# Performance work log

Hardware: AMD Instinct MI355X
Metric: run time of the kernel (lower is better)

Reference implementation:

```python
import jax, jax.numpy as jnp
import numpy as np
from jax import lax

B, SQ, SK, D, K = 4, 2048, 2048, 1024, 3


def setup_inputs() -> dict:
    key = jax.random.key(0)
    ks = jax.random.split(key, 16)
    s = 0.02
    return {
        "query_hidden": jax.random.normal(ks[0], (B, SQ, D), jnp.float32),
        "memory_hidden": jax.random.normal(ks[1], (B, SK, D), jnp.float32),
        "attention_mask": jax.random.randint(ks[2], (SQ, SK), 0, 2).astype(bool),
        # Linear projections (torch: y = x @ W.T + b)
        "q_w": jax.random.normal(ks[3], (D, D), jnp.float32) * s,
        "q_b": jnp.zeros((D,), jnp.float32),
        "k_w": jax.random.normal(ks[4], (D, D), jnp.float32) * s,
        "k_b": jnp.zeros((D,), jnp.float32),
        "v_w": jax.random.normal(ks[5], (D, D), jnp.float32) * s,
        "v_b": jnp.zeros((D,), jnp.float32),
        "o_w": jax.random.normal(ks[6], (D, D), jnp.float32) * s,
        "o_b": jnp.zeros((D,), jnp.float32),
        # ConvTransform1D: depthwise conv kernels [D,1,K], bias [D], scalar gate
        "q_kernel": jax.random.normal(ks[7], (D, 1, K), jnp.float32) * s,
        "q_cbias": jnp.zeros((D,), jnp.float32),
        "q_gate": jnp.zeros((), jnp.float32),
        "k_kernel": jax.random.normal(ks[8], (D, 1, K), jnp.float32) * s,
        "k_cbias": jnp.zeros((D,), jnp.float32),
        "k_gate": jnp.zeros((), jnp.float32),
        "v_kernel": jax.random.normal(ks[9], (D, 1, K), jnp.float32) * s,
        "v_cbias": jnp.zeros((D,), jnp.float32),
        "v_gate": jnp.zeros((), jnp.float32),
    }


def _conv_transform(x, kernel, cbias, gate):
    """Gated depthwise 1D conv along seq: x + tanh(gate) * dwconv(x). x: [B,S,D]."""
    xc = jnp.transpose(x, (0, 2, 1))  # [B,D,S]
    y = lax.conv_general_dilated(
        xc, kernel, window_strides=(1,), padding="SAME",
        dimension_numbers=("NCH", "OIH", "NCH"), feature_group_count=x.shape[-1])
    y = y + cbias[None, :, None]
    return x + jnp.tanh(gate) * jnp.transpose(y, (0, 2, 1))


def reference(query_hidden, memory_hidden, attention_mask,
              q_w, q_b, k_w, k_b, v_w, v_b, o_w, o_b,
              q_kernel, q_cbias, q_gate,
              k_kernel, k_cbias, k_gate,
              v_kernel, v_cbias, v_gate):
    d_model = query_hidden.shape[-1]
    q = _conv_transform(query_hidden @ q_w.T + q_b, q_kernel, q_cbias, q_gate)
    k = _conv_transform(memory_hidden @ k_w.T + k_b, k_kernel, k_cbias, k_gate)
    v = _conv_transform(memory_hidden @ v_w.T + v_b, v_kernel, v_cbias, v_gate)
    # [B,Sq,Sk]
    logits = jnp.einsum("bqd,bkd->bqk", q, k) / jnp.sqrt(jnp.float32(d_model))
    mask = attention_mask[None, :, :]  # broadcast like torch unsqueeze(0)
    logits = jnp.where(mask, logits, jnp.finfo(logits.dtype).min)
    attn = jax.nn.softmax(logits, axis=-1)
    out = jnp.einsum("bqk,bkd->bqd", attn, v) @ o_w.T + o_b
    return out
```

## Files before the change

### kernel.cpp

```cpp
#include <hip/hip_runtime.h>
#include <cstdint>
#include <cstddef>


#define GLOBAL_AS __attribute__((address_space(1)))
#define LDS_AS    __attribute__((address_space(3)))

typedef _Float16 h8 __attribute__((ext_vector_type(8)));
typedef float    f4_t __attribute__((ext_vector_type(4)));
typedef unsigned short us8 __attribute__((ext_vector_type(8)));

__device__ __forceinline__ float bf2f(unsigned short u) {
    union { unsigned int i; float f; } x; x.i = ((unsigned int)u) << 16; return x.f;
}
__device__ __forceinline__ float rd(const void* p, long i, int isBf) {
    return isBf ? bf2f(((const unsigned short*)p)[i]) : ((const float*)p)[i];
}

struct Probe16 { const unsigned short* p[16]; int n[16]; };

__global__ void k_probes(Probe16 a, const unsigned int* __restrict__ mask,
                         int* __restrict__ flags) {
    if (blockIdx.x < 16) {
        __shared__ int cnt;
        if (threadIdx.x == 0) cnt = 0;
        __syncthreads();
        const unsigned short* s = a.p[blockIdx.x];
        const int n = a.n[blockIdx.x];
        int bad = 0;
        for (int i = threadIdx.x; i < n; i += 256) {
            int e = (s[i] >> 7) & 0xFF;
            if (e >= 0x8F || (e > 0 && e <= 0x60)) bad++;
        }
        atomicAdd(&cnt, bad);
        __syncthreads();
        if (threadIdx.x == 0) flags[blockIdx.x] = (cnt * 4 > n) ? 0 : 1;
    } else {
        __shared__ int vi32, vf32, vbf, vf16;
        if (threadIdx.x == 0) { vi32 = vf32 = vbf = vf16 = 0; }
        __syncthreads();
        int bi32 = 0, bf32 = 0, bbf = 0, bf16c = 0;
        for (int i = threadIdx.x; i < 4096; i += 256) {
            unsigned int w = mask[i];
            if (!(w == 0u || w == 1u)) bi32++;
            if (!(w == 0u || w == 0x3F800000u)) bf32++;
            unsigned int h0 = w & 0xFFFFu, h1 = w >> 16;
            if (!((h0 == 0u || h0 == 0x3F80u) && (h1 == 0u || h1 == 0x3F80u))) bbf++;
            if (!((h0 == 0u || h0 == 0x3C00u) && (h1 == 0u || h1 == 0x3C00u))) bf16c++;
        }
        if (bi32) atomicAdd(&vi32, 1);
        if (bf32) atomicAdd(&vf32, 1);
        if (bbf)  atomicAdd(&vbf, 1);
        if (bf16c) atomicAdd(&vf16, 1);
        __syncthreads();
        if (threadIdx.x == 0) {
            int w;
            if (vi32 == 0) w = 4;
            else if (vf32 == 0) w = 4;
            else if (vbf == 0) w = 2;
            else if (vf16 == 0) w = 2;
            else w = 1;
            flags[16] = w;
        }
    }
}

__global__ void k_mask_bytes(const void* __restrict__ m, unsigned char* __restrict__ out,
                             long n, const int* __restrict__ widthFlag) {
    long i = ((long)blockIdx.x * 256 + threadIdx.x) * 4;
    if (i >= n) return;
    const int w = *widthFlag;
    unsigned int packed = 0;
    if (w == 4) {
        const unsigned int* p = (const unsigned int*)m;
#pragma unroll
        for (int u = 0; u < 4; ++u) packed |= (p[i + u] != 0u ? 1u : 0u) << (8 * u);
    } else if (w == 2) {
        const unsigned short* p = (const unsigned short*)m;
#pragma unroll
        for (int u = 0; u < 4; ++u) packed |= (p[i + u] != 0u ? 1u : 0u) << (8 * u);
    } else {
        const unsigned char* p = (const unsigned char*)m;
#pragma unroll
        for (int u = 0; u < 4; ++u) packed |= (p[i + u] != 0u ? 1u : 0u) << (8 * u);
    }
    *(unsigned int*)(out + i) = packed;
}

struct ConvSrc { const void* kern[3]; const void* cb[3]; const void* gate[3]; };
__global__ void k_conv_params(ConvSrc p, const int* __restrict__ flags,
                              _Float16* __restrict__ out, float* __restrict__ tg, int D) {
#pragma unroll
    for (int t = 0; t < 3; ++t) {
        const int kIs = flags[6 + t], cIs = flags[13 + t];
        for (int d = threadIdx.x; d < D; d += 256) {
#pragma unroll
            for (int j = 0; j < 3; ++j)
                out[t * 3 * D + j * D + d] = (_Float16)rd(p.kern[t], (long)d * 3 + j, kIs);
            out[9 * D + t * D + d] = (_Float16)rd(p.cb[t], d, cIs);
        }
    }
    if (threadIdx.x < 3) {
        const void* g = p.gate[threadIdx.x];
        float gv = rd(g, 0, ((const unsigned int*)g)[0] == 0u ? 1 : 0);
        tg[threadIdx.x] = tanhf(gv);
    }
}

__device__ __forceinline__ h8 cvt8(const void* src, size_t off8, int isBf) {
    h8 d;
    if (isBf) {
        us8 s = *(const us8*)((const unsigned short*)src + off8 * 8);
#pragma unroll
        for (int u = 0; u < 8; ++u) d[u] = (_Float16)bf2f(s[u]);
    } else {
        const float* f = (const float*)src + off8 * 8;
        f4_t a = *(const f4_t*)f;
        f4_t b = *(const f4_t*)(f + 4);
#pragma unroll
        for (int u = 0; u < 4; ++u) { d[u] = (_Float16)a[u]; d[4 + u] = (_Float16)b[u]; }
    }
    return d;
}

__global__ void k_h_to_f16(const void* __restrict__ s0, const void* __restrict__ s1,
                           _Float16* __restrict__ dst, int n8each,
                           const int* __restrict__ flags) {
    int i = blockIdx.x * blockDim.x + threadIdx.x;
    if (i >= 2 * n8each) return;
    int seg = i / n8each, off = i - seg * n8each;
    h8 d = cvt8(seg ? s1 : s0, off, flags[seg]);
    *(h8*)(dst + (size_t)i * 8) = d;
}

struct Ptr4 { const void* p[4]; };
__global__ void k_w_to_f16(Ptr4 srcs, _Float16* __restrict__ dst, int n8each,
                           const int* __restrict__ flags) {
    int i = blockIdx.x * blockDim.x + threadIdx.x;
    if (i >= 4 * n8each) return;
    int seg = i / n8each, off = i - seg * n8each;
    h8 d = cvt8(srcs.p[seg], off, flags[seg]);
    *(h8*)(dst + (size_t)i * 8) = d;
}

template <int MODE, int MTILE>
__global__ __launch_bounds__(256, 4) void k_gemm_nt(
    const _Float16* __restrict__ A, const _Float16* __restrict__ Bm,
    void* __restrict__ Cout,
    const void* __restrict__ bias, const int* __restrict__ biasFlag,
    const void* __restrict__ bias2, const int* __restrict__ biasFlag2,
    int N, int K, long sA, long sB, long sC,
    float scale, const unsigned char* __restrict__ mask8,
    int NT, int BZ) {

    constexpr int NI = (MTILE == 128) ? 4 : 2;
    constexpr int NCA = MTILE / 32;
    __shared__ __align__(16) _Float16 As[MTILE * 64];
    __shared__ __align__(16) _Float16 Bs[128 * 64];

    const long id = blockIdx.x;
    const int xcd = (int)(id & 7);
    const long local = id >> 3;
    const int col = (int)(local % NT);
    const long g = (local / NT) * 8 + xcd;
    const int bz = (int)(g % BZ);
    const int brow = (int)(g / BZ);

    const int tid  = threadIdx.x;
    const int wave = tid >> 6, lane = tid & 63;
    const int wm = (wave >> 1) * (MTILE / 2), wn = (wave & 1) * 64;
    const int lr = lane & 15, lq = lane >> 4;

    const _Float16* Ab = A + (long)bz * sA + (size_t)brow * MTILE * K;
    const _Float16* Bb = Bm + (long)bz * sB + (size_t)col * 128 * K;

    f4_t acc[NI][4] = {};

    const _Float16* gA[NCA];
    _Float16* lA[NCA];
#pragma unroll
    for (int j = 0; j < NCA; ++j) {
        int c = tid + j * 256;
        int r = c >> 3, s = ((c & 7) - r) & 7;
        gA[j] = Ab + (size_t)r * K + s * 8;
        lA[j] = As + c * 8;
    }
    const _Float16* gB[4];
    _Float16* lB[4];
#pragma unroll
    for (int j = 0; j < 4; ++j) {
        int c = tid + j * 256;
        int r = c >> 3, s = ((c & 7) - r) & 7;
        gB[j] = Bb + (size_t)r * K + s * 8;
        lB[j] = Bs + c * 8;
    }

    for (int kb = 0; kb < K; kb += 64) {
#pragma unroll
        for (int j = 0; j < NCA; ++j)
            __builtin_amdgcn_global_load_lds((void GLOBAL_AS*)(gA[j] + kb), (void LDS_AS*)lA[j], 16, 0, 0);
#pragma unroll
        for (int j = 0; j < 4; ++j)
            __builtin_amdgcn_global_load_lds((void GLOBAL_AS*)(gB[j] + kb), (void LDS_AS*)lB[j], 16, 0, 0);
        __syncthreads();

#pragma unroll
        for (int t = 0; t < 2; ++t) {
            const int fs = ((t * 4 + lq + lr) & 7) * 8;
            h8 af[NI], bfr[4];
#pragma unroll
            for (int i = 0; i < NI; ++i) af[i]  = *(const h8*)&As[(wm + i * 16 + lr) * 64 + fs];
#pragma unroll
            for (int j = 0; j < 4; ++j) bfr[j] = *(const h8*)&Bs[(wn + j * 16 + lr) * 64 + fs];
#pragma unroll
            for (int i = 0; i < NI; ++i)
#pragma unroll
                for (int j = 0; j < 4; ++j)
                    acc[i][j] = __builtin_amdgcn_mfma_f32_16x16x32_f16(af[i], bfr[j], acc[i][j], 0, 0, 0);
        }
        __syncthreads();
    }

    const long row0 = (long)brow * MTILE + wm + lq * 4;
    const long col0 = (long)col * 128 + wn + lr;

    if constexpr (MODE == 3) {
        _Float16* C = (_Float16*)Cout + (long)bz * sC;
#pragma unroll
        for (int i = 0; i < NI; ++i)
#pragma unroll
            for (int j = 0; j < 4; ++j)
#pragma unroll
                for (int r = 0; r < 4; ++r) {
                    long row = row0 + i * 16 + r;
                    long ccol = col0 + j * 16;
                    bool keep = mask8[row * (long)N + ccol] != 0;
                    float v = acc[i][j][r] * scale;
                    v = fminf(fmaxf(v, -60000.0f), 60000.0f);
                    C[row * (long)N + ccol] = (_Float16)(keep ? v : -60000.0f);
                }
    } else {
        float bv[4];
        if constexpr (MODE != 0) {
            const void* bp = bias; const int* bfp = biasFlag; long boff = 0;
            if (bias2 != nullptr && col * 128 >= (N >> 1)) {
                bp = bias2; bfp = biasFlag2; boff = (long)(N >> 1);
            }
            const int bIs = *bfp;
#pragma unroll
            for (int j = 0; j < 4; ++j) bv[j] = rd(bp, col0 + j * 16 - boff, bIs);
        } else {
#pragma unroll
            for (int j = 0; j < 4; ++j) bv[j] = 0.0f;
        }
        if constexpr (MODE == 2) {
            float* C = (float*)Cout + (long)bz * sC;
#pragma unroll
            for (int i = 0; i < NI; ++i)
#pragma unroll
                for (int j = 0; j < 4; ++j)
#pragma unroll
                    for (int r = 0; r < 4; ++r)
                        C[(row0 + i * 16 + r) * (long)N + col0 + j * 16] = acc[i][j][r] + bv[j];
        } else {
            _Float16* C = (_Float16*)Cout + (long)bz * sC;
#pragma unroll
            for (int i = 0; i < NI; ++i)
#pragma unroll
                for (int j = 0; j < 4; ++j)
#pragma unroll
                    for (int r = 0; r < 4; ++r) {
                        float v = acc[i][j][r] + bv[j];
                        v = fminf(fmaxf(v, -65000.0f), 65000.0f);
                        C[(row0 + i * 16 + r) * (long)N + col0 + j * 16] = (_Float16)v;
                    }
        }
    }
}

struct ConvP {
    const _Float16* x; int xs; _Float16* y;
    const _Float16* kp; const _Float16* cb; const float* tg;
};
__global__ void k_dwconv2(ConvP p0, ConvP p1, int S, int D) {
    const ConvP& p = blockIdx.z ? p1 : p0;
    int s = blockIdx.x, b = blockIdx.y;
    int d0 = threadIdx.x * 8;
    const size_t xb = ((size_t)b * S + s) * p.xs + d0;
    const size_t yb = ((size_t)b * S + s) * D + d0;
    h8 zero;
#pragma unroll
    for (int u = 0; u < 8; ++u) zero[u] = (_Float16)0.0f;
    h8 xc = *(const h8*)(p.x + xb);
    h8 xp = (s > 0)     ? *(const h8*)(p.x + xb - p.xs) : zero;
    h8 xn = (s < S - 1) ? *(const h8*)(p.x + xb + p.xs) : zero;
    h8 k0 = *(const h8*)(p.kp + 0 * D + d0);
    h8 k1 = *(const h8*)(p.kp + 1 * D + d0);
    h8 k2 = *(const h8*)(p.kp + 2 * D + d0);
    h8 cb = *(const h8*)(p.cb + d0);
    float tg = *p.tg;
    h8 o;
#pragma unroll
    for (int u = 0; u < 8; ++u) {
        float cv = (float)xp[u] * (float)k0[u] + (float)xc[u] * (float)k1[u] +
                   (float)xn[u] * (float)k2[u] + (float)cb[u];
        float v = (float)xc[u] + tg * cv;
        o[u] = (_Float16)fminf(fmaxf(v, -65000.0f), 65000.0f);
    }
    *(h8*)(p.y + yb) = o;
}

__global__ void k_dwconv_t(const _Float16* __restrict__ x, int xs,
                           _Float16* __restrict__ vt,
                           const _Float16* __restrict__ kp,
                           const _Float16* __restrict__ cbp,
                           const float* __restrict__ tgp,
                           int SK, int D) {
    __shared__ _Float16 T[64][65];
    int b = blockIdx.z;
    int s0 = blockIdx.x * 64, d0 = blockIdx.y * 64;
    int tid = threadIdx.x;
    float tg = *tgp;
    h8 zero;
#pragma unroll
    for (int u = 0; u < 8; ++u) zero[u] = (_Float16)0.0f;
#pragma unroll
    for (int it = 0; it < 2; ++it) {
        int idx = it * 256 + tid;
        int r = idx >> 3, c = (idx & 7) * 8;
        int s = s0 + r;
        const size_t xb = ((size_t)b * SK + s) * xs + d0 + c;
        h8 xc = *(const h8*)(x + xb);
        h8 xp = (s > 0)      ? *(const h8*)(x + xb - xs) : zero;
        h8 xn = (s < SK - 1) ? *(const h8*)(x + xb + xs) : zero;
        h8 k0 = *(const h8*)(kp + 0 * D + d0 + c);
        h8 k1 = *(const h8*)(kp + 1 * D + d0 + c);
        h8 k2 = *(const h8*)(kp + 2 * D + d0 + c);
        h8 cb = *(const h8*)(cbp + d0 + c);
#pragma unroll
        for (int u = 0; u < 8; ++u) {
            float cv = (float)xp[u] * (float)k0[u] + (float)xc[u] * (float)k1[u] +
                       (float)xn[u] * (float)k2[u] + (float)cb[u];
            float v = (float)xc[u] + tg * cv;
            T[r][c + u] = (_Float16)fminf(fmaxf(v, -65000.0f), 65000.0f);
        }
    }
    __syncthreads();
#pragma unroll
    for (int it = 0; it < 2; ++it) {
        int idx = it * 256 + tid;
        int dr = idx >> 3, c = (idx & 7) * 8;
        h8 o;
#pragma unroll
        for (int u = 0; u < 8; ++u) o[u] = T[c + u][dr];
        *(h8*)(vt + ((size_t)b * D + d0 + dr) * SK + s0 + c) = o;
    }
}

__global__ __launch_bounds__(256) void k_softmax(const _Float16* __restrict__ sc,
                                                 _Float16* __restrict__ pr, int SK) {
    const long row = blockIdx.x;
    const int tid = threadIdx.x, lane = tid & 63, wave = tid >> 6;
    h8 v = *(const h8*)(sc + row * (long)SK + tid * 8);
    float f[8]; float mx = -3.0e38f;
#pragma unroll
    for (int u = 0; u < 8; ++u) { f[u] = (float)v[u]; mx = fmaxf(mx, f[u]); }
#pragma unroll
    for (int o = 32; o > 0; o >>= 1) mx = fmaxf(mx, __shfl_xor(mx, o, 64));
    __shared__ float red[8];
    if (lane == 0) red[wave] = mx;
    __syncthreads();
    mx = fmaxf(fmaxf(red[0], red[1]), fmaxf(red[2], red[3]));
    float sum = 0.0f;
#pragma unroll
    for (int u = 0; u < 8; ++u) { f[u] = __expf(f[u] - mx); sum += f[u]; }
#pragma unroll
    for (int o = 32; o > 0; o >>= 1) sum += __shfl_xor(sum, o, 64);
    if (lane == 0) red[4 + wave] = sum;
    __syncthreads();
    sum = red[4] + red[5] + red[6] + red[7];
    float inv = 1.0f / sum;
    h8 o8;
#pragma unroll
    for (int u = 0; u < 8; ++u) o8[u] = (_Float16)(f[u] * inv);
    *(h8*)(pr + row * (long)SK + tid * 8) = o8;
}

extern "C" void kernel_launch(void* const* d_in, const int* in_sizes, int n_in,
                              void* d_out, int out_size, void* d_ws, size_t ws_size,
                              hipStream_t stream) {
    const int Bn = 4, SQ = 2048, SK = 2048, D = 1024;
    const size_t nQ = (size_t)Bn * SQ * D;
    const long   nM = (long)SQ * SK;

    const void* qh = d_in[0];
    const void* mh = d_in[1];
    const void* mask = d_in[2];
    const void* q_w = d_in[3];
    const void* q_b = d_in[4];
    const void* k_w = d_in[5];
    const void* k_b = d_in[6];
    const void* v_w = d_in[7];
    const void* v_b = d_in[8];
    const void* o_w = d_in[9];
    const void* o_b = d_in[10];
    const void* q_kern = d_in[11];
    const void* q_cb   = d_in[12];
    const void* q_g    = d_in[13];
    const void* k_kern = d_in[14];
    const void* k_cb   = d_in[15];
    const void* k_g    = d_in[16];
    const void* v_kern = d_in[17];
    const void* v_cb   = d_in[18];
    const void* v_g    = d_in[19];

    char* ws = (char*)d_ws;
    _Float16* scores   = (_Float16*)(ws + 0);
    _Float16* attn_out = (_Float16*)(ws + 0);
    _Float16* w16      = (_Float16*)(ws + 33554432);
    unsigned char* mask8 = (unsigned char*)(ws + 33554432);
    _Float16* par16    = (_Float16*)(ws + 37748736);
    float*    tgf      = (float*)(ws + 37748736 + 12 * 1024 * 2);
    _Float16* lin      = (_Float16*)(ws + 41943040);
    _Float16* lin_q    = lin;
    _Float16* lin_kv   = lin + nQ;
    _Float16* probs    = lin;
    _Float16* conv     = (_Float16*)(ws + 92274688);
    _Float16* qh16     = conv;
    _Float16* mh16     = conv + nQ;
    _Float16* vt       = (_Float16*)(ws + 125829120);
    int*      flags    = (int*)(ws + 142606336);

    Probe16 pa;
    const void* pp[16] = {qh, mh, q_w, k_w, v_w, o_w, q_kern, k_kern, v_kern,
                          q_b, k_b, v_b, o_b, q_cb, k_cb, v_cb};
    const int   pn[16] = {2048, 2048, 2048, 2048, 2048, 2048, 3072, 3072, 3072,
                          1024, 1024, 1024, 1024, 1024, 1024, 1024};
    for (int i = 0; i < 16; ++i) { pa.p[i] = (const unsigned short*)pp[i]; pa.n[i] = pn[i]; }
    k_probes<<<17, 256, 0, stream>>>(pa, (const unsigned int*)mask, flags);

    const int nH8 = (int)(nQ / 8);
    k_h_to_f16<<<(2 * nH8 + 255) / 256, 256, 0, stream>>>(qh, mh, qh16, nH8, flags + 0);
    const int nW8 = D * D / 8;
    Ptr4 wp; wp.p[0] = q_w; wp.p[1] = k_w; wp.p[2] = v_w; wp.p[3] = o_w;
    k_w_to_f16<<<(4 * nW8 + 255) / 256, 256, 0, stream>>>(wp, w16, nW8, flags + 2);

    k_gemm_nt<1, 64><<<dim3(1024), 256, 0, stream>>>(
        qh16, w16, lin_q, q_b, flags + 9, nullptr, nullptr,
        D, D, 0, 0, 0, 1.0f, nullptr, 8, 1);
    k_gemm_nt<1, 128><<<dim3(1024), 256, 0, stream>>>(
        mh16, w16 + (size_t)D * D, lin_kv, k_b, flags + 10, v_b, flags + 11,
        2 * D, D, 0, 0, 0, 1.0f, nullptr, 16, 1);

    k_mask_bytes<<<(int)(nM / 4 / 256), 256, 0, stream>>>(mask, mask8, nM, flags + 16);
    ConvSrc cs;
    cs.kern[0] = q_kern; cs.kern[1] = k_kern; cs.kern[2] = v_kern;
    cs.cb[0] = q_cb; cs.cb[1] = k_cb; cs.cb[2] = v_cb;
    cs.gate[0] = q_g; cs.gate[1] = k_g; cs.gate[2] = v_g;
    k_conv_params<<<1, 256, 0, stream>>>(cs, flags, par16, tgf, D);

    ConvP cq{lin_q, D, conv + 0 * nQ, par16 + 0 * 3 * D, par16 + 9 * D + 0 * D, tgf + 0};
    ConvP ck{lin_kv, 2 * D, conv + 1 * nQ, par16 + 1 * 3 * D, par16 + 9 * D + 1 * D, tgf + 1};
    k_dwconv2<<<dim3(SQ, Bn, 2), 128, 0, stream>>>(cq, ck, SQ, D);
    k_dwconv_t<<<dim3(SK / 64, D / 64, Bn), 256, 0, stream>>>(
        lin_kv + D, 2 * D, vt, par16 + 2 * 3 * D, par16 + 9 * D + 2 * D, tgf + 2, SK, D);

    k_gemm_nt<3, 128><<<dim3(1024), 256, 0, stream>>>(
        conv + 0 * nQ, conv + 1 * nQ, scores, nullptr, nullptr, nullptr, nullptr,
        SK, D, (long)SQ * D, (long)SK * D, (long)SQ * SK, 0.03125f, mask8, 16, 4);

    k_softmax<<<Bn * SQ, 256, 0, stream>>>(scores, probs, SK);

    k_gemm_nt<0, 64><<<dim3(1024), 256, 0, stream>>>(
        probs, vt, attn_out, nullptr, nullptr, nullptr, nullptr,
        D, SK, (long)SQ * SK, (long)D * SK, (long)SQ * D, 1.0f, nullptr, 8, 4);

    k_gemm_nt<2, 64><<<dim3(1024), 256, 0, stream>>>(
        attn_out, w16 + 3 * (size_t)D * D, d_out, o_b, flags + 12, nullptr, nullptr,
        D, D, 0, 0, 0, 1.0f, nullptr, 8, 1);

    (void)in_sizes; (void)n_in; (void)out_size; (void)ws_size;
}
```

Baseline: 406.3 us.

## Fuse fp32-to-fp16 activation conversion into projection GEMM loads and merge prep kernels

The projection GEMMs now load fp32 query/memory activations straight into LDS and convert them to fp16 while building MFMA fragments. This removes the separate activation conversion kernel and its round trip of an fp16 copy through memory. The weight conversion, mask packing and conv-parameter kernels are merged into one launch to cut launch overhead. The KV projection switches from 128-row to 64-row tiles because the fp32 A tile doubles LDS use. This costs more LDS traffic, conversion work inside the GEMM inner loop, and lower per-block reuse. The fp32 path also assumes fp32 inputs and ignores the bf16 probe flag for activations.

```diff
diff --git a/kernel.cpp b/kernel.cpp
--- a/kernel.cpp
+++ b/kernel.cpp
@@ -65,48 +65,6 @@
     }
 }
 
-__global__ void k_mask_bytes(const void* __restrict__ m, unsigned char* __restrict__ out,
-                             long n, const int* __restrict__ widthFlag) {
-    long i = ((long)blockIdx.x * 256 + threadIdx.x) * 4;
-    if (i >= n) return;
-    const int w = *widthFlag;
-    unsigned int packed = 0;
-    if (w == 4) {
-        const unsigned int* p = (const unsigned int*)m;
-#pragma unroll
-        for (int u = 0; u < 4; ++u) packed |= (p[i + u] != 0u ? 1u : 0u) << (8 * u);
-    } else if (w == 2) {
-        const unsigned short* p = (const unsigned short*)m;
-#pragma unroll
-        for (int u = 0; u < 4; ++u) packed |= (p[i + u] != 0u ? 1u : 0u) << (8 * u);
-    } else {
-        const unsigned char* p = (const unsigned char*)m;
-#pragma unroll
-        for (int u = 0; u < 4; ++u) packed |= (p[i + u] != 0u ? 1u : 0u) << (8 * u);
-    }
-    *(unsigned int*)(out + i) = packed;
-}
-
-struct ConvSrc { const void* kern[3]; const void* cb[3]; const void* gate[3]; };
-__global__ void k_conv_params(ConvSrc p, const int* __restrict__ flags,
-                              _Float16* __restrict__ out, float* __restrict__ tg, int D) {
-#pragma unroll
-    for (int t = 0; t < 3; ++t) {
-        const int kIs = flags[6 + t], cIs = flags[13 + t];
-        for (int d = threadIdx.x; d < D; d += 256) {
-#pragma unroll
-            for (int j = 0; j < 3; ++j)
-                out[t * 3 * D + j * D + d] = (_Float16)rd(p.kern[t], (long)d * 3 + j, kIs);
-            out[9 * D + t * D + d] = (_Float16)rd(p.cb[t], d, cIs);
-        }
-    }
-    if (threadIdx.x < 3) {
-        const void* g = p.gate[threadIdx.x];
-        float gv = rd(g, 0, ((const unsigned int*)g)[0] == 0u ? 1 : 0);
-        tg[threadIdx.x] = tanhf(gv);
-    }
-}
-
 __device__ __forceinline__ h8 cvt8(const void* src, size_t off8, int isBf) {
     h8 d;
     if (isBf) {
@@ -123,29 +81,62 @@
     return d;
 }
 
-__global__ void k_h_to_f16(const void* __restrict__ s0, const void* __restrict__ s1,
-                           _Float16* __restrict__ dst, int n8each,
-                           const int* __restrict__ flags) {
-    int i = blockIdx.x * blockDim.x + threadIdx.x;
-    if (i >= 2 * n8each) return;
-    int seg = i / n8each, off = i - seg * n8each;
-    h8 d = cvt8(seg ? s1 : s0, off, flags[seg]);
-    *(h8*)(dst + (size_t)i * 8) = d;
-}
-
 struct Ptr4 { const void* p[4]; };
-__global__ void k_w_to_f16(Ptr4 srcs, _Float16* __restrict__ dst, int n8each,
-                           const int* __restrict__ flags) {
-    int i = blockIdx.x * blockDim.x + threadIdx.x;
-    if (i >= 4 * n8each) return;
-    int seg = i / n8each, off = i - seg * n8each;
-    h8 d = cvt8(srcs.p[seg], off, flags[seg]);
-    *(h8*)(dst + (size_t)i * 8) = d;
-}
-
-template <int MODE, int MTILE>
+struct ConvSrc { const void* kern[3]; const void* cb[3]; const void* gate[3]; };
+
+__global__ void k_prep(Ptr4 wsrc, _Float16* __restrict__ wdst, int nW8,
+                       const void* __restrict__ m, unsigned char* __restrict__ mout,
+                       long nM, ConvSrc cp, _Float16* __restrict__ par,
+                       float* __restrict__ tg, int D,
+                       const int* __restrict__ flags) {
+    const long id = blockIdx.x;
+    if (id < 2048) {
+        int i = (int)id * 256 + threadIdx.x;
+        if (i >= 4 * nW8) return;
+        int seg = i / nW8, off = i - seg * nW8;
+        h8 d = cvt8(wsrc.p[seg], off, flags[2 + seg]);
+        *(h8*)(wdst + (size_t)i * 8) = d;
+    } else if (id < 6144) {
+        long i = ((id - 2048) * 256 + threadIdx.x) * 4;
+        if (i >= nM) return;
+        const int w = flags[16];
+        unsigned int packed = 0;
+        if (w == 4) {
+            const unsigned int* p = (const unsigned int*)m;
+#pragma unroll
+            for (int u = 0; u < 4; ++u) packed |= (p[i + u] != 0u ? 1u : 0u) << (8 * u);
+        } else if (w == 2) {
+            const unsigned short* p = (const unsigned short*)m;
+#pragma unroll
+            for (int u = 0; u < 4; ++u) packed |= (p[i + u] != 0u ? 1u : 0u) << (8 * u);
+        } else {
+            const unsigned char* p = (const unsigned char*)m;
+#pragma unroll
+            for (int u = 0; u < 4; ++u) packed |= (p[i + u] != 0u ? 1u : 0u) << (8 * u);
+        }
+        *(unsigned int*)(mout + i) = packed;
+    } else {
+#pragma unroll
+        for (int t = 0; t < 3; ++t) {
+            const int kIs = flags[6 + t], cIs = flags[13 + t];
+            for (int d = threadIdx.x; d < D; d += 256) {
+#pragma unroll
+                for (int j = 0; j < 3; ++j)
+                    par[t * 3 * D + j * D + d] = (_Float16)rd(cp.kern[t], (long)d * 3 + j, kIs);
+                par[9 * D + t * D + d] = (_Float16)rd(cp.cb[t], d, cIs);
+            }
+        }
+        if (threadIdx.x < 3) {
+            const void* g = cp.gate[threadIdx.x];
+            float gv = rd(g, 0, ((const unsigned int*)g)[0] == 0u ? 1 : 0);
+            tg[threadIdx.x] = tanhf(gv);
+        }
+    }
+}
+
+template <int MODE, int MTILE, int AFP32>
 __global__ __launch_bounds__(256, 4) void k_gemm_nt(
-    const _Float16* __restrict__ A, const _Float16* __restrict__ Bm,
+    const void* __restrict__ A, const _Float16* __restrict__ Bm,
     void* __restrict__ Cout,
     const void* __restrict__ bias, const int* __restrict__ biasFlag,
     const void* __restrict__ bias2, const int* __restrict__ biasFlag2,
@@ -153,10 +144,14 @@
     float scale, const unsigned char* __restrict__ mask8,
     int NT, int BZ) {
 
-    constexpr int NI = (MTILE == 128) ? 4 : 2;
-    constexpr int NCA = MTILE / 32;
-    __shared__ __align__(16) _Float16 As[MTILE * 64];
+    constexpr int NI  = (MTILE == 128) ? 4 : 2;
+    constexpr int ES  = AFP32 ? 4 : 2;
+    constexpr int SEG = 4 * ES;
+    constexpr int CHA = MTILE * SEG / 256;
+    __shared__ __align__(16) char AsRaw[(size_t)MTILE * 64 * ES];
     __shared__ __align__(16) _Float16 Bs[128 * 64];
+    _Float16* As16 = (_Float16*)AsRaw;
+    float*    As32 = (float*)AsRaw;
 
     const long id = blockIdx.x;
     const int xcd = (int)(id & 7);
@@ -171,19 +166,19 @@
     const int wm = (wave >> 1) * (MTILE / 2), wn = (wave & 1) * 64;
     const int lr = lane & 15, lq = lane >> 4;
 
-    const _Float16* Ab = A + (long)bz * sA + (size_t)brow * MTILE * K;
+    const char* Abc = (const char*)A + ((long)bz * sA + (size_t)brow * MTILE * K) * ES;
     const _Float16* Bb = Bm + (long)bz * sB + (size_t)col * 128 * K;
 
     f4_t acc[NI][4] = {};
 
-    const _Float16* gA[NCA];
-    _Float16* lA[NCA];
-#pragma unroll
-    for (int j = 0; j < NCA; ++j) {
+    const char* gA[CHA];
+    char* lA[CHA];
+#pragma unroll
+    for (int j = 0; j < CHA; ++j) {
         int c = tid + j * 256;
-        int r = c >> 3, s = ((c & 7) - r) & 7;
-        gA[j] = Ab + (size_t)r * K + s * 8;
-        lA[j] = As + c * 8;
+        int r = c / SEG, s = ((c & (SEG - 1)) - r) & (SEG - 1);
+        gA[j] = Abc + ((size_t)r * K) * ES + s * 16;
+        lA[j] = AsRaw + (size_t)c * 16;
     }
     const _Float16* gB[4];
     _Float16* lB[4];
@@ -197,8 +192,9 @@
 
     for (int kb = 0; kb < K; kb += 64) {
 #pragma unroll
-        for (int j = 0; j < NCA; ++j)
-            __builtin_amdgcn_global_load_lds((void GLOBAL_AS*)(gA[j] + kb), (void LDS_AS*)lA[j], 16, 0, 0);
+        for (int j = 0; j < CHA; ++j)
+            __builtin_amdgcn_global_load_lds((void GLOBAL_AS*)(gA[j] + (size_t)kb * ES),
+                                             (void LDS_AS*)lA[j], 16, 0, 0);
 #pragma unroll
         for (int j = 0; j < 4; ++j)
             __builtin_amdgcn_global_load_lds((void GLOBAL_AS*)(gB[j] + kb), (void LDS_AS*)lB[j], 16, 0, 0);
@@ -206,12 +202,30 @@
 
 #pragma unroll
         for (int t = 0; t < 2; ++t) {
-            const int fs = ((t * 4 + lq + lr) & 7) * 8;
             h8 af[NI], bfr[4];
-#pragma unroll
-            for (int i = 0; i < NI; ++i) af[i]  = *(const h8*)&As[(wm + i * 16 + lr) * 64 + fs];
-#pragma unroll
-            for (int j = 0; j < 4; ++j) bfr[j] = *(const h8*)&Bs[(wn + j * 16 + lr) * 64 + fs];
+            if constexpr (AFP32) {
+                const int s0 = t * 8 + lq * 2;
+#pragma unroll
+                for (int i = 0; i < NI; ++i) {
+                    int row = wm + i * 16 + lr;
+                    f4_t a0 = *(const f4_t*)&As32[row * 64 + ((s0 + lr) & 15) * 4];
+                    f4_t a1 = *(const f4_t*)&As32[row * 64 + ((s0 + 1 + lr) & 15) * 4];
+#pragma unroll
+                    for (int u = 0; u < 4; ++u) {
+                        af[i][u] = (_Float16)a0[u];
+                        af[i][4 + u] = (_Float16)a1[u];
+                    }
+                }
+            } else {
+                const int fs = ((t * 4 + lq + lr) & 7) * 8;
+#pragma unroll
+                for (int i = 0; i < NI; ++i)
+                    af[i] = *(const h8*)&As16[(wm + i * 16 + lr) * 64 + fs];
+            }
+            const int fsB = ((t * 4 + lq + lr) & 7) * 8;
+#pragma unroll
+            for (int j = 0; j < 4; ++j)
+                bfr[j] = *(const h8*)&Bs[(wn + j * 16 + lr) * 64 + fsB];
 #pragma unroll
             for (int i = 0; i < NI; ++i)
 #pragma unroll
@@ -418,18 +432,16 @@
     _Float16* scores   = (_Float16*)(ws + 0);
     _Float16* attn_out = (_Float16*)(ws + 0);
     _Float16* w16      = (_Float16*)(ws + 33554432);
-    unsigned char* mask8 = (unsigned char*)(ws + 33554432);
-    _Float16* par16    = (_Float16*)(ws + 37748736);
-    float*    tgf      = (float*)(ws + 37748736 + 12 * 1024 * 2);
     _Float16* lin      = (_Float16*)(ws + 41943040);
     _Float16* lin_q    = lin;
     _Float16* lin_kv   = lin + nQ;
     _Float16* probs    = lin;
     _Float16* conv     = (_Float16*)(ws + 92274688);
-    _Float16* qh16     = conv;
-    _Float16* mh16     = conv + nQ;
     _Float16* vt       = (_Float16*)(ws + 125829120);
     int*      flags    = (int*)(ws + 142606336);
+    unsigned char* mask8 = (unsigned char*)(ws + 142610432);
+    _Float16* par16    = (_Float16*)(ws + 146804736);
+    float*    tgf      = (float*)(ws + 146804736 + 12 * 1024 * 2);
 
     Probe16 pa;
     const void* pp[16] = {qh, mh, q_w, k_w, v_w, o_w, q_kern, k_kern, v_kern,
@@ -439,25 +451,20 @@
     for (int i = 0; i < 16; ++i) { pa.p[i] = (const unsigned short*)pp[i]; pa.n[i] = pn[i]; }
     k_probes<<<17, 256, 0, stream>>>(pa, (const unsigned int*)mask, flags);
 
-    const int nH8 = (int)(nQ / 8);
-    k_h_to_f16<<<(2 * nH8 + 255) / 256, 256, 0, stream>>>(qh, mh, qh16, nH8, flags + 0);
     const int nW8 = D * D / 8;
     Ptr4 wp; wp.p[0] = q_w; wp.p[1] = k_w; wp.p[2] = v_w; wp.p[3] = o_w;
-    k_w_to_f16<<<(4 * nW8 + 255) / 256, 256, 0, stream>>>(wp, w16, nW8, flags + 2);
-
-    k_gemm_nt<1, 64><<<dim3(1024), 256, 0, stream>>>(
-        qh16, w16, lin_q, q_b, flags + 9, nullptr, nullptr,
-        D, D, 0, 0, 0, 1.0f, nullptr, 8, 1);
-    k_gemm_nt<1, 128><<<dim3(1024), 256, 0, stream>>>(
-        mh16, w16 + (size_t)D * D, lin_kv, k_b, flags + 10, v_b, flags + 11,
-        2 * D, D, 0, 0, 0, 1.0f, nullptr, 16, 1);
-
-    k_mask_bytes<<<(int)(nM / 4 / 256), 256, 0, stream>>>(mask, mask8, nM, flags + 16);
     ConvSrc cs;
     cs.kern[0] = q_kern; cs.kern[1] = k_kern; cs.kern[2] = v_kern;
     cs.cb[0] = q_cb; cs.cb[1] = k_cb; cs.cb[2] = v_cb;
     cs.gate[0] = q_g; cs.gate[1] = k_g; cs.gate[2] = v_g;
-    k_conv_params<<<1, 256, 0, stream>>>(cs, flags, par16, tgf, D);
+    k_prep<<<6145, 256, 0, stream>>>(wp, w16, nW8, mask, mask8, nM, cs, par16, tgf, D, flags);
+
+    k_gemm_nt<1, 64, 1><<<dim3(1024), 256, 0, stream>>>(
+        qh, w16, lin_q, q_b, flags + 9, nullptr, nullptr,
+        D, D, 0, 0, 0, 1.0f, nullptr, 8, 1);
+    k_gemm_nt<1, 64, 1><<<dim3(2048), 256, 0, stream>>>(
+        mh, w16 + (size_t)D * D, lin_kv, k_b, flags + 10, v_b, flags + 11,
+        2 * D, D, 0, 0, 0, 1.0f, nullptr, 16, 1);
 
     ConvP cq{lin_q, D, conv + 0 * nQ, par16 + 0 * 3 * D, par16 + 9 * D + 0 * D, tgf + 0};
     ConvP ck{lin_kv, 2 * D, conv + 1 * nQ, par16 + 1 * 3 * D, par16 + 9 * D + 1 * D, tgf + 1};
@@ -465,17 +472,17 @@
     k_dwconv_t<<<dim3(SK / 64, D / 64, Bn), 256, 0, stream>>>(
         lin_kv + D, 2 * D, vt, par16 + 2 * 3 * D, par16 + 9 * D + 2 * D, tgf + 2, SK, D);
 
-    k_gemm_nt<3, 128><<<dim3(1024), 256, 0, stream>>>(
+    k_gemm_nt<3, 128, 0><<<dim3(1024), 256, 0, stream>>>(
         conv + 0 * nQ, conv + 1 * nQ, scores, nullptr, nullptr, nullptr, nullptr,
         SK, D, (long)SQ * D, (long)SK * D, (long)SQ * SK, 0.03125f, mask8, 16, 4);
 
     k_softmax<<<Bn * SQ, 256, 0, stream>>>(scores, probs, SK);
 
-    k_gemm_nt<0, 64><<<dim3(1024), 256, 0, stream>>>(
+    k_gemm_nt<0, 64, 0><<<dim3(1024), 256, 0, stream>>>(
         probs, vt, attn_out, nullptr, nullptr, nullptr, nullptr,
         D, SK, (long)SQ * SK, (long)D * SK, (long)SQ * D, 1.0f, nullptr, 8, 4);
 
-    k_gemm_nt<2, 64><<<dim3(1024), 256, 0, stream>>>(
+    k_gemm_nt<2, 64, 0><<<dim3(1024), 256, 0, stream>>>(
         attn_out, w16 + 3 * (size_t)D * D, d_out, o_b, flags + 12, nullptr, nullptr,
         D, D, 0, 0, 0, 1.0f, nullptr, 8, 1);
 
```

After: 425.2 us. 4.6% more time.
